# Performance work log

Hardware: AMD Instinct MI355X
Metric: run time of the kernel (lower is better)

## Reference

```python
import jax, jax.numpy as jnp
import numpy as np

N_DENSE = 13
N_SPARSE = 26
VOCAB = 100000
EMB = 64
BATCH = 16384


def setup_inputs() -> dict:
    key = jax.random.key(0)
    ks = jax.random.split(key, 8)
    sparse_inputs = jax.random.randint(ks[0], (BATCH, N_SPARSE), 0, VOCAB, dtype=jnp.int32)
    dense_inputs = jax.random.normal(ks[1], (BATCH, N_DENSE), dtype=jnp.float32)
    # embedding tables (all fields share vocab size -> stacked [F, V, D])
    emb1 = jax.random.normal(ks[2], (N_SPARSE, VOCAB, 1), dtype=jnp.float32) * 0.05
    emb2 = jax.random.normal(ks[3], (N_SPARSE, VOCAB, EMB), dtype=jnp.float32) * 0.05
    # linear dense layer [13 -> 1]
    W_dense = jax.random.normal(ks[4], (N_DENSE, 1), dtype=jnp.float32) * 0.1
    b_dense = jnp.zeros((1,), dtype=jnp.float32)
    # finish / like heads [1 -> 1] with sigmoid
    W_finish = jax.random.normal(ks[5], (1, 1), dtype=jnp.float32)
    b_finish = jnp.zeros((1,), dtype=jnp.float32)
    W_like = jax.random.normal(ks[6], (1, 1), dtype=jnp.float32)
    b_like = jnp.zeros((1,), dtype=jnp.float32)
    return dict(sparse_inputs=sparse_inputs, dense_inputs=dense_inputs,
                emb1=emb1, emb2=emb2, W_dense=W_dense, b_dense=b_dense,
                W_finish=W_finish, b_finish=b_finish, W_like=W_like, b_like=b_like)


def reference(sparse_inputs, dense_inputs, emb1, emb2, W_dense, b_dense,
              W_finish, b_finish, W_like, b_like):
    F = emb2.shape[0]
    fields = jnp.arange(F)[None, :]  # [1, F] broadcast over batch
    # first order: dense linear + sum of per-field scalar embeddings
    linear_dense_out = dense_inputs @ W_dense + b_dense            # [B, 1]
    lin_sparse = emb1[fields, sparse_inputs, 0]                    # [B, F]
    first_order = linear_dense_out + jnp.sum(lin_sparse, axis=1, keepdims=True)
    # second order: FM sum-square trick
    embeddings = emb2[fields, sparse_inputs]                       # [B, F, E]
    summed = jnp.sum(embeddings, axis=1)                           # [B, E]
    squared_sum = summed * summed
    squared = jnp.sum(embeddings * embeddings, axis=1)             # [B, E]
    second_order = 0.5 * jnp.sum(squared_sum - squared, axis=1, keepdims=True)
    logits = first_order + second_order                            # [B, 1]
    finish = jax.nn.sigmoid(logits @ W_finish + b_finish)
    like = jax.nn.sigmoid(logits @ W_like + b_like)
    return finish, like
```

## Files before the change

kernel.cpp:

```cpp
#include <hip/hip_runtime.h>
#include <math.h>

#define BATCH    16384
#define N_SPARSE 26
#define N_DENSE  13
#define VOCAB    100000
#define EMB      64

__global__ __launch_bounds__(256) void fm_mtl_kernel(
    const int*   __restrict__ sparse,
    const float* __restrict__ dense,
    const float* __restrict__ emb1,
    const float* __restrict__ emb2,
    const float* __restrict__ W_dense,
    const float* __restrict__ b_dense,
    const float* __restrict__ W_finish,
    const float* __restrict__ b_finish,
    const float* __restrict__ W_like,
    const float* __restrict__ b_like,
    float*       __restrict__ out)
{
    const int gtid = blockIdx.x * blockDim.x + threadIdx.x;
    const int row  = gtid >> 6;
    const int lane = threadIdx.x & 63;
    if (row >= BATCH) return;

    int   idx_f       = 0;
    float scalar_part = 0.0f;
    if (lane < N_SPARSE) {
        idx_f       = sparse[row * N_SPARSE + lane];
        scalar_part = emb1[lane * VOCAB + idx_f];
    }
    if (lane < N_DENSE) {
        scalar_part += dense[row * N_DENSE + lane] * W_dense[lane];
    }

    float sum_e   = 0.0f;
    float sumsq_e = 0.0f;
    #pragma unroll
    for (int f = 0; f < N_SPARSE; ++f) {
        int idx = __shfl(idx_f, f);
        float v = emb2[((size_t)f * VOCAB + (size_t)idx) * EMB + lane];
        sum_e   += v;
        sumsq_e += v * v;
    }

    float val = 0.5f * (sum_e * sum_e - sumsq_e) + scalar_part;

    #pragma unroll
    for (int off = 32; off > 0; off >>= 1)
        val += __shfl_down(val, off);

    if (lane == 0) {
        float logits = val + b_dense[0];
        float zf = logits * W_finish[0] + b_finish[0];
        float zl = logits * W_like[0]   + b_like[0];
        out[row]         = 1.0f / (1.0f + __expf(-zf));
        out[BATCH + row] = 1.0f / (1.0f + __expf(-zl));
    }
}

extern "C" void kernel_launch(void* const* d_in, const int* in_sizes, int n_in,
                              void* d_out, int out_size, void* d_ws, size_t ws_size,
                              hipStream_t stream) {
    const int*   sparse   = (const int*)  d_in[0];
    const float* dense    = (const float*)d_in[1];
    const float* emb1     = (const float*)d_in[2];
    const float* emb2     = (const float*)d_in[3];
    const float* W_dense  = (const float*)d_in[4];
    const float* b_dense  = (const float*)d_in[5];
    const float* W_finish = (const float*)d_in[6];
    const float* b_finish = (const float*)d_in[7];
    const float* W_like   = (const float*)d_in[8];
    const float* b_like   = (const float*)d_in[9];
    float* out = (float*)d_out;

    const int threads = 256;
    const int blocks  = (BATCH * 64) / threads;
    fm_mtl_kernel<<<blocks, threads, 0, stream>>>(
        sparse, dense, emb1, emb2,
        W_dense, b_dense, W_finish, b_finish, W_like, b_like, out);
}
```

Measured before the change: 744.9 us.

## Process four rows per wavefront with float4 embedding gathers

Each 64-lane wavefront now handles four batch rows, with 16 lanes per row, and each lane loads a float4 of the 64-wide embedding row instead of one scalar. The sparse indices and emb1 lookups are split across 13 lanes as two halves, and the reduction shrinks to a 16-lane xor shuffle. The aim is fewer, wider memory instructions and four times fewer waves for the random-gather-bound workload, at the cost of more complex lane indexing.

```diff
diff --git a/kernel.cpp b/kernel.cpp
--- a/kernel.cpp
+++ b/kernel.cpp
@@ -21,40 +21,53 @@
     float*       __restrict__ out)
 {
     const int gtid = blockIdx.x * blockDim.x + threadIdx.x;
-    const int row  = gtid >> 6;
+    const int wave = gtid >> 6;
     const int lane = threadIdx.x & 63;
+    const int g    = lane >> 4;
+    const int m    = lane & 15;
+    const int row  = wave * 4 + g;
     if (row >= BATCH) return;
 
-    int   idx_f       = 0;
-    float scalar_part = 0.0f;
-    if (lane < N_SPARSE) {
-        idx_f       = sparse[row * N_SPARSE + lane];
-        scalar_part = emb1[lane * VOCAB + idx_f];
-    }
-    if (lane < N_DENSE) {
-        scalar_part += dense[row * N_DENSE + lane] * W_dense[lane];
+    int idx_a = 0, idx_b = 0;
+    if (m < N_DENSE) {
+        idx_a = sparse[row * N_SPARSE + m];
+        idx_b = sparse[row * N_SPARSE + 13 + m];
     }
 
-    float sum_e   = 0.0f;
-    float sumsq_e = 0.0f;
+    float first = 0.0f;
+    if (m < N_DENSE) {
+        first  = emb1[m * VOCAB + idx_a];
+        first += emb1[(13 + m) * VOCAB + idx_b];
+        first += dense[row * N_DENSE + m] * W_dense[m];
+    }
+
+    float4 s = make_float4(0.f, 0.f, 0.f, 0.f);
+    float4 q = make_float4(0.f, 0.f, 0.f, 0.f);
     #pragma unroll
     for (int f = 0; f < N_SPARSE; ++f) {
-        int idx = __shfl(idx_f, f);
-        float v = emb2[((size_t)f * VOCAB + (size_t)idx) * EMB + lane];
-        sum_e   += v;
-        sumsq_e += v * v;
+        const int src = (lane & 48) | (f < 13 ? f : f - 13);
+        const int idx = __shfl((f < 13) ? idx_a : idx_b, src);
+        const float4* p = (const float4*)(emb2 +
+                            ((size_t)f * VOCAB + (size_t)idx) * EMB);
+        const float4 v = p[m];
+        s.x += v.x; s.y += v.y; s.z += v.z; s.w += v.w;
+        q.x = fmaf(v.x, v.x, q.x);
+        q.y = fmaf(v.y, v.y, q.y);
+        q.z = fmaf(v.z, v.z, q.z);
+        q.w = fmaf(v.w, v.w, q.w);
     }
 
-    float val = 0.5f * (sum_e * sum_e - sumsq_e) + scalar_part;
+    float partial = 0.5f * ((s.x * s.x - q.x) + (s.y * s.y - q.y) +
+                            (s.z * s.z - q.z) + (s.w * s.w - q.w)) + first;
 
     #pragma unroll
-    for (int off = 32; off > 0; off >>= 1)
-        val += __shfl_down(val, off);
+    for (int off = 8; off > 0; off >>= 1)
+        partial += __shfl_xor(partial, off);
 
-    if (lane == 0) {
-        float logits = val + b_dense[0];
-        float zf = logits * W_finish[0] + b_finish[0];
-        float zl = logits * W_like[0]   + b_like[0];
+    if (m == 0) {
+        const float logits = partial + b_dense[0];
+        const float zf = fmaf(logits, W_finish[0], b_finish[0]);
+        const float zl = fmaf(logits, W_like[0],   b_like[0]);
         out[row]         = 1.0f / (1.0f + __expf(-zf));
         out[BATCH + row] = 1.0f / (1.0f + __expf(-zl));
     }
@@ -76,7 +89,7 @@
     float* out = (float*)d_out;
 
     const int threads = 256;
-    const int blocks  = (BATCH * 64) / threads;
+    const int blocks  = (BATCH / 4) * 64 / threads;
     fm_mtl_kernel<<<blocks, threads, 0, stream>>>(
         sparse, dense, emb1, emb2,
         W_dense, b_dense, W_finish, b_finish, W_like, b_like, out);
```

After: 743.9 us. About the same (-0.1%).
